# Kernel optimization log

Hardware: AMD Instinct MI355X
Metric: run time of the kernel (lower is better)

## Reference

```python
import jax, jax.numpy as jnp
import numpy as np
from jax import lax

NUM_NODES = 100000
FEAT = 256
RANK = 16
NNZ = 4000000
NUM_HE = 125000  # num_hyperedges == num_edges_total
K = 2000000      # int(0.5 * NNZ)


def setup_inputs() -> dict:
    key = jax.random.key(0)
    ks = jax.random.split(key, 6)
    x = jax.random.normal(ks[0], (NUM_NODES, FEAT), dtype=jnp.float32)
    W = jax.random.normal(ks[1], (RANK, FEAT), dtype=jnp.float32)
    edge_factors = jax.random.normal(ks[2], (NUM_HE, RANK), dtype=jnp.float32)
    V_idx = jax.random.randint(ks[3], (NNZ,), 0, NUM_NODES, dtype=jnp.int32)
    E_idx = jax.random.randint(ks[4], (NNZ,), 0, NUM_HE, dtype=jnp.int32)
    edge_ids = jax.random.randint(ks[5], (NUM_HE,), 0, NUM_HE, dtype=jnp.int32)
    return {"x": x, "W": W, "edge_factors": edge_factors,
            "V_idx": V_idx, "E_idx": E_idx, "edge_ids": edge_ids, "k": K}


def _segment_mean(vals, seg_ids, num_segments):
    s = jax.ops.segment_sum(vals, seg_ids, num_segments=num_segments)
    c = jax.ops.segment_sum(jnp.ones_like(vals), seg_ids, num_segments=num_segments)
    return s / jnp.maximum(c, 1.0)


def reference(x, W, edge_factors, V_idx, E_idx, edge_ids, k):
    # node_proj(x): [N, rank]; gather per-incidence node and edge factors, dot product
    proj = x @ W.T                                  # [N, rank]
    ef = edge_factors[edge_ids[E_idx]]              # [nnz, rank]
    logits = jnp.sum(proj[V_idx] * ef, axis=-1)     # [nnz]
    scores = jax.nn.sigmoid(logits)

    # is_test=True path: deterministic top-k keep set
    _, keep_ids = lax.top_k(scores, k)
    hard = jnp.zeros_like(scores).at[keep_ids].set(1.0)
    # straight-through: forward == hard, gradient flows through scores where hard==1
    soft = hard + (scores - lax.stop_gradient(scores)) * hard

    edge_probs = _segment_mean(lax.stop_gradient(scores), E_idx, NUM_HE)
    edge_soft = _segment_mean(soft, E_idx, NUM_HE)
    edge_hard = (_segment_mean(hard, E_idx, NUM_HE) > 0).astype(jnp.float32)
    return scores, soft, hard, edge_probs, edge_soft, edge_hard
```

## Files before the change

### kernel.cpp

```cpp
#include <hip/hip_runtime.h>
#include <math.h>

#define FEAT 256
#define RANKK 16
#define CAND_CAP 131072
#define TIE_CAP 2048
#define NBK_MAX 512
#define PB_CHUNK 8192
#define SPLIT 4
#define PRJ_NODES 64

typedef unsigned long long u64;

static __device__ __forceinline__ u64 pack_pair(unsigned e_low, unsigned bits, unsigned idx) {
    return ((u64)e_low << 56) | ((u64)bits << 26) | (u64)idx;
}

static __device__ __forceinline__ u64 pack_v(unsigned v, unsigned idx, unsigned e_low) {
    return ((u64)v << 40) | ((u64)idx << 8) | (u64)e_low;
}

__global__ __launch_bounds__(256) void ehist_scan(const int* __restrict__ E_idx,
        unsigned* __restrict__ bucketCnt, unsigned* __restrict__ bucketBase,
        unsigned* __restrict__ cursor, unsigned* __restrict__ ticket, int nnz) {
    __shared__ unsigned h[NBK_MAX];
    __shared__ unsigned ps[256];
    __shared__ unsigned isLast;
    int t = threadIdx.x;
    for (int j = t; j < NBK_MAX; j += 256) h[j] = 0;
    __syncthreads();
    for (int i = blockIdx.x * 256 + t; i < nnz; i += gridDim.x * 256)
        atomicAdd(&h[((unsigned)E_idx[i]) >> 8], 1u);
    __syncthreads();
    for (int j = t; j < NBK_MAX; j += 256)
        if (h[j]) atomicAdd(&bucketCnt[j], h[j]);
    __threadfence();
    if (t == 0) isLast = (atomicAdd(ticket, 1u) == gridDim.x - 1) ? 1u : 0u;
    __syncthreads();
    if (!isLast) return;
    unsigned a0 = atomicAdd(&bucketCnt[2 * t], 0u);
    unsigned a1 = atomicAdd(&bucketCnt[2 * t + 1], 0u);
    unsigned pairsum = a0 + a1;
    ps[t] = pairsum;
    __syncthreads();
    for (int off = 1; off < 256; off <<= 1) {
        unsigned v = (t >= off) ? ps[t - off] : 0u;
        __syncthreads();
        ps[t] += v;
        __syncthreads();
    }
    unsigned excl = ps[t] - pairsum;
    bucketBase[2 * t] = excl;           cursor[2 * t] = excl;
    bucketBase[2 * t + 1] = excl + a0;  cursor[2 * t + 1] = excl + a0;
    if (t == 255) bucketBase[NBK_MAX] = ps[255];
}

__global__ __launch_bounds__(256) void prep_combo(
        const float4* __restrict__ ef, const int* __restrict__ edge_ids,
        float4* __restrict__ ef2, int nhe,
        const float* __restrict__ x, const float* __restrict__ Wm,
        float* __restrict__ proj, int n_nodes, int G) {
    __shared__ float Ws[RANKK][FEAT + 4];
    __shared__ float Xs[PRJ_NODES][128 + 4];
    if ((int)blockIdx.x < G) {
        int t = blockIdx.x * 256 + threadIdx.x;
        if (t < nhe * 4) {
            int e = t >> 2, c = t & 3;
            ef2[(size_t)e * 4 + c] = ef[(size_t)edge_ids[e] * 4 + c];
        }
        return;
    }
    int pb = blockIdx.x - G;
    const float4* x4 = (const float4*)x;
    const float4* w4 = (const float4*)Wm;
    for (int i = threadIdx.x; i < RANKK * 64; i += 256) {
        int r = i >> 6, c4 = i & 63;
        *(float4*)&Ws[r][c4 * 4] = w4[(size_t)r * 64 + c4];
    }
    int nodeBase = pb * PRJ_NODES;
    int np = threadIdx.x >> 3;
    int rp = threadIdx.x & 7;
    int n0 = np * 2, r0 = rp * 2;
    double a00 = 0.0, a01 = 0.0, a10 = 0.0, a11 = 0.0;
    for (int chunk = 0; chunk < 2; ++chunk) {
        __syncthreads();
        for (int i = threadIdx.x; i < PRJ_NODES * 32; i += 256) {
            int row = i >> 5, c4 = i & 31;
            int node = nodeBase + row;
            float4 v = make_float4(0.f, 0.f, 0.f, 0.f);
            if (node < n_nodes) v = x4[(size_t)node * 64 + chunk * 32 + c4];
            *(float4*)&Xs[row][c4 * 4] = v;
        }
        __syncthreads();
        int jw = chunk * 128;
        #pragma unroll 8
        for (int j4 = 0; j4 < 32; ++j4) {
            float4 xa = *(const float4*)&Xs[n0][j4 * 4];
            float4 xb = *(const float4*)&Xs[n0 + 1][j4 * 4];
            float4 wa = *(const float4*)&Ws[r0][jw + j4 * 4];
            float4 wb = *(const float4*)&Ws[r0 + 1][jw + j4 * 4];
            a00 += (double)xa.x * wa.x + (double)xa.y * wa.y + (double)xa.z * wa.z + (double)xa.w * wa.w;
            a01 += (double)xa.x * wb.x + (double)xa.y * wb.y + (double)xa.z * wb.z + (double)xa.w * wb.w;
            a10 += (double)xb.x * wa.x + (double)xb.y * wa.y + (double)xb.z * wa.z + (double)xb.w * wa.w;
            a11 += (double)xb.x * wb.x + (double)xb.y * wb.y + (double)xb.z * wb.z + (double)xb.w * wb.w;
        }
    }
    int nodeA = nodeBase + n0;
    int nodeB = nodeA + 1;
    if (nodeA < n_nodes) {
        proj[(size_t)nodeA * RANKK + r0]     = (float)a00;
        proj[(size_t)nodeA * RANKK + r0 + 1] = (float)a01;
    }
    if (nodeB < n_nodes) {
        proj[(size_t)nodeB * RANKK + r0]     = (float)a10;
        proj[(size_t)nodeB * RANKK + r0 + 1] = (float)a11;
    }
}

__global__ __launch_bounds__(256) void sort_kernel(const int* __restrict__ V_idx,
        const int* __restrict__ E_idx, u64* __restrict__ vlist,
        unsigned* __restrict__ cursor, int nnz, int nb) {
    __shared__ unsigned bh[NBK_MAX];
    int t = threadIdx.x;
    for (int j = t; j < NBK_MAX; j += 256) bh[j] = 0;
    __syncthreads();
    int base = blockIdx.x * PB_CHUNK;
    int nE = nnz - base;
    if (nE > PB_CHUNK) nE = PB_CHUNK;
    for (int o = t; o < nE; o += 256)
        atomicAdd(&bh[((unsigned)E_idx[base + o]) >> 8], 1u);
    __syncthreads();
    for (int b = t; b < nb; b += 256) {
        unsigned c = bh[b];
        bh[b] = c ? atomicAdd(&cursor[b], c) : 0u;
    }
    __syncthreads();
    for (int o = t; o < nE; o += 256) {
        int i = base + o;
        unsigned e = (unsigned)E_idx[i];
        unsigned v = (unsigned)V_idx[i];
        unsigned pos = atomicAdd(&bh[e >> 8], 1u);
        vlist[pos] = pack_v(v, (unsigned)i, e & 255u);
    }
}

__global__ __launch_bounds__(256) void bucket_score(
        const float4* __restrict__ proj4, const float4* __restrict__ ef4,
        const unsigned* __restrict__ bucketBase, u64* __restrict__ list,
        float* __restrict__ scores, int nhe) {
    __shared__ float efs[256][20];
    int t = threadIdx.x;
    int b = blockIdx.x >> 2;
    int part = blockIdx.x & (SPLIT - 1);
    for (int jj = t; jj < 1024; jj += 256) {
        int edge = (b << 8) + (jj >> 2);
        if (edge < nhe) {
            float4 v = ef4[(size_t)edge * 4 + (jj & 3)];
            *(float4*)&efs[jj >> 2][(jj & 3) * 4] = v;
        }
    }
    __syncthreads();
    unsigned n0 = bucketBase[b], n1 = bucketBase[b + 1];
    #pragma unroll 2
    for (unsigned j = n0 + (part << 8) + t; j < n1; j += SPLIT * 256) {
        u64 p = list[j];
        unsigned v   = (unsigned)(p >> 40);
        unsigned idx = (unsigned)(p >> 8) & 0xFFFFFFu;
        unsigned el  = (unsigned)(p & 255u);
        float4 p0 = proj4[(size_t)v * 4 + 0];
        float4 p1 = proj4[(size_t)v * 4 + 1];
        float4 p2 = proj4[(size_t)v * 4 + 2];
        float4 p3 = proj4[(size_t)v * 4 + 3];
        float4 f0 = *(const float4*)&efs[el][0];
        float4 f1 = *(const float4*)&efs[el][4];
        float4 f2 = *(const float4*)&efs[el][8];
        float4 f3 = *(const float4*)&efs[el][12];
        double acc = (double)p0.x * f0.x + (double)p0.y * f0.y + (double)p0.z * f0.z + (double)p0.w * f0.w
                   + (double)p1.x * f1.x + (double)p1.y * f1.y + (double)p1.z * f1.z + (double)p1.w * f1.w
                   + (double)p2.x * f2.x + (double)p2.y * f2.y + (double)p2.z * f2.z + (double)p2.w * f2.w
                   + (double)p3.x * f3.x + (double)p3.y * f3.y + (double)p3.z * f3.z + (double)p3.w * f3.w;
        float s = (float)(1.0 / (1.0 + exp(-acc)));
        scores[idx] = s;
        list[j] = pack_pair(el, __float_as_uint(s), idx);
    }
}

__global__ __launch_bounds__(256) void score_linear(
        const float4* __restrict__ proj4, const float4* __restrict__ ef4,
        const int* __restrict__ V_idx, const int* __restrict__ E_idx,
        float* __restrict__ scores, int nnz) {
    int stride = gridDim.x * blockDim.x;
    #pragma unroll 2
    for (int i = blockIdx.x * blockDim.x + threadIdx.x; i < nnz; i += stride) {
        int v = V_idx[i], e = E_idx[i];
        float4 p0 = proj4[(size_t)v * 4 + 0];
        float4 p1 = proj4[(size_t)v * 4 + 1];
        float4 p2 = proj4[(size_t)v * 4 + 2];
        float4 p3 = proj4[(size_t)v * 4 + 3];
        float4 f0 = ef4[(size_t)e * 4 + 0];
        float4 f1 = ef4[(size_t)e * 4 + 1];
        float4 f2 = ef4[(size_t)e * 4 + 2];
        float4 f3 = ef4[(size_t)e * 4 + 3];
        double acc = (double)p0.x * f0.x + (double)p0.y * f0.y + (double)p0.z * f0.z + (double)p0.w * f0.w
                   + (double)p1.x * f1.x + (double)p1.y * f1.y + (double)p1.z * f1.z + (double)p1.w * f1.w
                   + (double)p2.x * f2.x + (double)p2.y * f2.y + (double)p2.z * f2.z + (double)p2.w * f2.w
                   + (double)p3.x * f3.x + (double)p3.y * f3.y + (double)p3.z * f3.z + (double)p3.w * f3.w;
        scores[i] = (float)(1.0 / (1.0 + exp(-acc)));
    }
}

__global__ __launch_bounds__(256) void pair_build(const int* __restrict__ E_idx,
        const float* __restrict__ scores, u64* __restrict__ pairs,
        unsigned* __restrict__ cursor, int nnz, int nb) {
    __shared__ unsigned bh[NBK_MAX];
    for (int t = threadIdx.x; t < NBK_MAX; t += 256) bh[t] = 0;
    __syncthreads();
    int base = blockIdx.x * PB_CHUNK;
    int nE = nnz - base;
    if (nE > PB_CHUNK) nE = PB_CHUNK;
    for (int o = threadIdx.x; o < nE; o += 256)
        atomicAdd(&bh[((unsigned)E_idx[base + o]) >> 8], 1u);
    __syncthreads();
    for (int b = threadIdx.x; b < nb; b += 256) {
        unsigned c = bh[b];
        bh[b] = c ? atomicAdd(&cursor[b], c) : 0u;
    }
    __syncthreads();
    for (int o = threadIdx.x; o < nE; o += 256) {
        int i = base + o;
        unsigned e = (unsigned)E_idx[i];
        unsigned bits = __float_as_uint(scores[i]);
        unsigned pos = atomicAdd(&bh[e >> 8], 1u);
        pairs[pos] = pack_pair(e & 255u, bits, (unsigned)i);
    }
}

__global__ void hist1_kernel(const float4* __restrict__ scores4, unsigned* __restrict__ hist1g,
                             int n4, int nnz) {
    __shared__ unsigned h[4096];
    for (int t = threadIdx.x; t < 4096; t += blockDim.x) h[t] = 0;
    __syncthreads();
    unsigned r1016 = 0, r1015 = 0, r0 = 0;
    int stride = gridDim.x * blockDim.x;
    for (int i = blockIdx.x * blockDim.x + threadIdx.x; i < n4; i += stride) {
        float4 sv = scores4[i];
        unsigned bb[4] = {__float_as_uint(sv.x), __float_as_uint(sv.y),
                          __float_as_uint(sv.z), __float_as_uint(sv.w)};
        #pragma unroll
        for (int q = 0; q < 4; ++q) {
            unsigned b = bb[q] >> 20;
            if (b == 1016) ++r1016;
            else if (b == 1015) ++r1015;
            else if (b == 0) ++r0;
            else atomicAdd(&h[b], 1u);
        }
    }
    for (int i = n4 * 4 + blockIdx.x * blockDim.x + threadIdx.x; i < nnz; i += stride) {
        unsigned b = __float_as_uint(((const float*)scores4)[i]) >> 20;
        if (b == 1016) ++r1016;
        else if (b == 1015) ++r1015;
        else if (b == 0) ++r0;
        else atomicAdd(&h[b], 1u);
    }
    if (r1016) atomicAdd(&h[1016], r1016);
    if (r1015) atomicAdd(&h[1015], r1015);
    if (r0) atomicAdd(&h[0], r0);
    __syncthreads();
    for (int t = threadIdx.x; t < 4096; t += blockDim.x)
        if (h[t]) atomicAdd(&hist1g[t], h[t]);
}

__global__ void scan1_kernel(const unsigned* __restrict__ hist,
                             unsigned* __restrict__ sel, const int* __restrict__ kptr) {
    __shared__ unsigned sfx[256];
    int t = threadIdx.x;
    unsigned local[16];
    unsigned s = 0;
    #pragma unroll
    for (int j = 0; j < 16; ++j) { local[j] = hist[t * 16 + j]; s += local[j]; }
    sfx[t] = s;
    __syncthreads();
    for (int off = 1; off < 256; off <<= 1) {
        unsigned add = (t + off < 256) ? sfx[t + off] : 0;
        __syncthreads();
        sfx[t] += add;
        __syncthreads();
    }
    unsigned krem = (unsigned)(*kptr);
    unsigned above = (t + 1 < 256) ? sfx[t + 1] : 0;
    if (above < krem && sfx[t] >= krem) {
        unsigned cum = above;
        int b = t * 16;
        for (int j = 15; j >= 0; --j) {
            unsigned cc = local[j];
            if (cum + cc >= krem) { b = t * 16 + j; break; }
            cum += cc;
        }
        sel[0] = krem - cum;
        sel[1] = ((unsigned)b) << 20;
    }
}

__global__ void compact_kernel(const float4* __restrict__ scores4,
                               const unsigned* __restrict__ sel,
                               uint2* __restrict__ cand, unsigned* __restrict__ candCount,
                               int n4, int nnz) {
    unsigned pref = sel[1] >> 20;
    int tid = blockIdx.x * blockDim.x + threadIdx.x;
    int stride = gridDim.x * blockDim.x;
    int lane = threadIdx.x & 63;
    int niter = (n4 + stride - 1) / stride;
    for (int kk = 0; kk < niter; ++kk) {
        int i = tid + kk * stride;
        bool inb = (i < n4);
        float4 sv = make_float4(0.f, 0.f, 0.f, 0.f);
        if (inb) sv = scores4[i];
        unsigned bb[4] = {__float_as_uint(sv.x), __float_as_uint(sv.y),
                          __float_as_uint(sv.z), __float_as_uint(sv.w)};
        #pragma unroll
        for (int q = 0; q < 4; ++q) {
            bool pred = inb && ((bb[q] >> 20) == pref);
            unsigned long long mask = __ballot(pred);
            if (mask) {
                int leader = __ffsll(mask) - 1;
                unsigned base = 0;
                if (lane == leader) base = atomicAdd(candCount, (unsigned)__popcll(mask));
                base = __shfl(base, leader, 64);
                if (pred) {
                    unsigned rank = __popcll(mask & ((1ull << lane) - 1ull));
                    unsigned pos = base + rank;
                    if (pos < CAND_CAP) cand[pos] = make_uint2(bb[q], (unsigned)(i * 4 + q));
                }
            }
        }
    }
    for (int i = n4 * 4 + tid; i < nnz; i += stride) {
        unsigned b = __float_as_uint(((const float*)scores4)[i]);
        if ((b >> 20) == pref) {
            unsigned pos = atomicAdd(candCount, 1u);
            if (pos < CAND_CAP) cand[pos] = make_uint2(b, (unsigned)i);
        }
    }
}

__global__ __launch_bounds__(256) void select_small(const uint2* __restrict__ cand,
                            const unsigned* __restrict__ candCount,
                            unsigned* __restrict__ sel, unsigned* __restrict__ tieList) {
    __shared__ unsigned h2[4096];
    __shared__ unsigned sfx[256];
    __shared__ unsigned sB2, sKrem2, sT, sM;
    __shared__ unsigned h3[256];
    __shared__ unsigned ties[TIE_CAP];
    __shared__ unsigned tcnt;
    int t = threadIdx.x;
    unsigned nc = *candCount;
    int n = (nc < CAND_CAP) ? (int)nc : CAND_CAP;
    unsigned krem = sel[0];
    unsigned pref = sel[1];

    for (int j = t; j < 4096; j += 256) h2[j] = 0;
    if (t == 0) tcnt = 0;
    __syncthreads();
    for (int j = t; j < n; j += 256) atomicAdd(&h2[(cand[j].x >> 8) & 0xFFF], 1u);
    __syncthreads();

    unsigned local[16];
    unsigned s = 0;
    #pragma unroll
    for (int j = 0; j < 16; ++j) { local[j] = h2[t * 16 + j]; s += local[j]; }
    sfx[t] = s;
    __syncthreads();
    for (int off = 1; off < 256; off <<= 1) {
        unsigned add = (t + off < 256) ? sfx[t + off] : 0;
        __syncthreads();
        sfx[t] += add;
        __syncthreads();
    }
    {
        unsigned above = (t + 1 < 256) ? sfx[t + 1] : 0;
        if (above < krem && sfx[t] >= krem) {
            unsigned cum = above;
            int b = t * 16;
            for (int j = 15; j >= 0; --j) {
                unsigned cc = local[j];
                if (cum + cc >= krem) { b = t * 16 + j; break; }
                cum += cc;
            }
            sB2 = (unsigned)b;
            sKrem2 = krem - cum;
        }
    }
    __syncthreads();

    h3[t] = 0;
    __syncthreads();
    unsigned b2 = sB2;
    for (int j = t; j < n; j += 256) {
        unsigned x = cand[j].x;
        if (((x >> 8) & 0xFFF) == b2) atomicAdd(&h3[x & 0xFF], 1u);
    }
    __syncthreads();
    sfx[t] = h3[t];
    __syncthreads();
    for (int off = 1; off < 256; off <<= 1) {
        unsigned add = (t + off < 256) ? sfx[t + off] : 0;
        __syncthreads();
        sfx[t] += add;
        __syncthreads();
    }
    {
        unsigned krem2 = sKrem2;
        unsigned above = (t + 1 < 256) ? sfx[t + 1] : 0;
        if (above < krem2 && sfx[t] >= krem2) {
            sT = pref | (b2 << 8) | (unsigned)t;
            sM = krem2 - above;
        }
    }
    __syncthreads();

    unsigned T = sT;
    for (int j = t; j < n; j += 256) {
        if (cand[j].x == T) {
            unsigned p = atomicAdd(&tcnt, 1u);
            if (p < TIE_CAP) ties[p] = cand[j].y;
        }
    }
    __syncthreads();
    if (t == 0) {
        unsigned cnt = (tcnt < TIE_CAP) ? tcnt : TIE_CAP;
        for (unsigned a = 1; a < cnt; ++a) {
            unsigned key = ties[a];
            int bpos = (int)a - 1;
            while (bpos >= 0 && ties[bpos] > key) { ties[bpos + 1] = ties[bpos]; --bpos; }
            ties[bpos + 1] = key;
        }
        unsigned m = sM;
        if (m > cnt) m = cnt;
        sel[2] = T;
        sel[3] = m;
        for (unsigned j = 0; j < m; ++j) tieList[j] = ties[j];
    }
}

__global__ __launch_bounds__(256) void edge_final(const u64* __restrict__ pairs,
        const unsigned* __restrict__ bucketBase, const unsigned* __restrict__ sel,
        const unsigned* __restrict__ tieList,
        float* __restrict__ eprob, float* __restrict__ esoft, float* __restrict__ ehard,
        int nhe) {
    __shared__ float ss[256];
    __shared__ unsigned cc[256];
    __shared__ unsigned hh[256];
    __shared__ unsigned ties[TIE_CAP];
    unsigned T = sel[2];
    unsigned m = sel[3];
    if (m > TIE_CAP) m = TIE_CAP;
    int t = threadIdx.x;
    ss[t] = 0.f; cc[t] = 0u; hh[t] = 0u;
    for (int j = t; j < (int)m; j += 256) ties[j] = tieList[j];
    __syncthreads();
    int b = blockIdx.x;
    unsigned n0 = bucketBase[b], n1 = bucketBase[b + 1];
    for (unsigned j = n0 + t; j < n1; j += 256) {
        u64 p = pairs[j];
        unsigned el = (unsigned)(p >> 56);
        unsigned bits = (unsigned)(p >> 26) & 0x3FFFFFFFu;
        atomicAdd(&ss[el], __uint_as_float(bits));
        atomicAdd(&cc[el], 1u);
        bool keep = bits > T;
        if (bits == T) {
            unsigned idx = (unsigned)(p & 0x3FFFFFFu);
            int lo = 0, hi = (int)m - 1;
            keep = false;
            while (lo <= hi) {
                int mid = (lo + hi) >> 1;
                unsigned v = ties[mid];
                if (v == idx) { keep = true; break; }
                if (v < idx) lo = mid + 1; else hi = mid - 1;
            }
        }
        if (keep) atomicAdd(&hh[el], 1u);
    }
    __syncthreads();
    int e = b * 256 + t;
    if (e < nhe) {
        float c = fmaxf((float)cc[t], 1.0f);
        eprob[e] = ss[t] / c;
        esoft[e] = (float)hh[t] / c;
        ehard[e] = (hh[t] > 0) ? 1.0f : 0.0f;
    }
}

__global__ __launch_bounds__(256) void write_hard(const float4* __restrict__ scores4,
                           const unsigned* __restrict__ sel,
                           const unsigned* __restrict__ tieList,
                           float4* __restrict__ hard4, float4* __restrict__ soft4,
                           int n4, int nnz) {
    __shared__ unsigned ties[TIE_CAP];
    unsigned T = sel[2];
    unsigned m = sel[3];
    if (m > TIE_CAP) m = TIE_CAP;
    for (int j = threadIdx.x; j < (int)m; j += blockDim.x) ties[j] = tieList[j];
    __syncthreads();
    int tid = blockIdx.x * blockDim.x + threadIdx.x;
    int stride = gridDim.x * blockDim.x;
    for (int i = tid; i < n4; i += stride) {
        float4 sv = scores4[i];
        unsigned bb[4] = {__float_as_uint(sv.x), __float_as_uint(sv.y),
                          __float_as_uint(sv.z), __float_as_uint(sv.w)};
        float hv[4];
        #pragma unroll
        for (int q = 0; q < 4; ++q) {
            bool keep = (bb[q] > T);
            if (bb[q] == T) {
                unsigned idx = (unsigned)(i * 4 + q);
                int lo = 0, hi = (int)m - 1;
                keep = false;
                while (lo <= hi) {
                    int mid = (lo + hi) >> 1;
                    unsigned v = ties[mid];
                    if (v == idx) { keep = true; break; }
                    if (v < idx) lo = mid + 1; else hi = mid - 1;
                }
            }
            hv[q] = keep ? 1.0f : 0.0f;
        }
        float4 outv = make_float4(hv[0], hv[1], hv[2], hv[3]);
        hard4[i] = outv;
        soft4[i] = outv;
    }
    const float* sc = (const float*)scores4;
    float* hard = (float*)hard4;
    float* soft = (float*)soft4;
    for (int i = n4 * 4 + tid; i < nnz; i += stride) {
        unsigned b = __float_as_uint(sc[i]);
        bool keep = (b > T);
        if (b == T) {
            unsigned idx = (unsigned)i;
            int lo = 0, hi = (int)m - 1;
            keep = false;
            while (lo <= hi) {
                int mid = (lo + hi) >> 1;
                unsigned v = ties[mid];
                if (v == idx) { keep = true; break; }
                if (v < idx) lo = mid + 1; else hi = mid - 1;
            }
        }
        float hvv = keep ? 1.0f : 0.0f;
        hard[i] = hvv;
        soft[i] = hvv;
    }
}

extern "C" void kernel_launch(void* const* d_in, const int* in_sizes, int n_in,
                              void* d_out, int out_size, void* d_ws, size_t ws_size,
                              hipStream_t stream) {
    const float* x        = (const float*)d_in[0];
    const float* Wm       = (const float*)d_in[1];
    const float* ef       = (const float*)d_in[2];
    const int*   V_idx    = (const int*)d_in[3];
    const int*   E_idx    = (const int*)d_in[4];
    const int*   edge_ids = (const int*)d_in[5];
    const int*   kptr     = (const int*)d_in[6];

    const int nnz     = in_sizes[3];
    const int nhe     = in_sizes[5];
    const int n_nodes = in_sizes[0] / FEAT;
    const int nb      = (nhe + 255) >> 8;

    float* out    = (float*)d_out;
    float* scores = out;
    float* soft   = out + (size_t)nnz;
    float* hard   = out + 2 * (size_t)nnz;
    float* eprob  = out + 3 * (size_t)nnz;
    float* esoft  = eprob + nhe;
    float* ehard  = esoft + nhe;

    u64*   vlist = (u64*)soft;
    uint2* cand  = (uint2*)eprob;

    char* w = (char*)d_ws;
    unsigned* hist1      = (unsigned*)w;
    unsigned* bucketCnt  = hist1 + 4096;
    unsigned* candCount  = bucketCnt + NBK_MAX;
    unsigned* ticket1    = candCount + 1;
    unsigned* sel        = ticket1 + 1;
    unsigned* tieList    = sel + 8;
    unsigned* bucketBase = tieList + TIE_CAP;
    unsigned* cursor     = bucketBase + NBK_MAX + 1;
    char* auxEnd = (char*)(cursor + NBK_MAX);
    size_t auxAligned = (((size_t)(auxEnd - w)) + 255) & ~(size_t)255;
    size_t zeroBytes = (size_t)(4096 + NBK_MAX + 2) * sizeof(unsigned);

    size_t ef2Bytes  = (size_t)nhe * RANKK * sizeof(float);
    size_t projBytes = (size_t)n_nodes * RANKK * sizeof(float);

    bool wsBig = (ws_size >= auxAligned + ef2Bytes + projBytes);
    float* ef2;
    float* proj;
    if (wsBig) {
        ef2  = (float*)(w + auxAligned);
        proj = (float*)(w + auxAligned + ef2Bytes);
    } else {
        ef2  = hard;
        proj = hard + (size_t)nhe * RANKK;
    }

    hipMemsetAsync(w, 0, zeroBytes, stream);

    ehist_scan<<<128, 256, 0, stream>>>(E_idx, bucketCnt, bucketBase, cursor, ticket1, nnz);

    int G = (nhe * 4 + 255) / 256;
    int P = (n_nodes + PRJ_NODES - 1) / PRJ_NODES;
    prep_combo<<<G + P, 256, 0, stream>>>((const float4*)ef, edge_ids, (float4*)ef2, nhe,
                                          x, Wm, proj, n_nodes, G);

    int nChunks = (nnz + PB_CHUNK - 1) / PB_CHUNK;
    if (wsBig) {
        sort_kernel<<<nChunks, 256, 0, stream>>>(V_idx, E_idx, vlist, cursor, nnz, nb);
        bucket_score<<<nb * SPLIT, 256, 0, stream>>>(
            (const float4*)proj, (const float4*)ef2, bucketBase, vlist, scores, nhe);
    } else {
        score_linear<<<2048, 256, 0, stream>>>(
            (const float4*)proj, (const float4*)ef2, V_idx, E_idx, scores, nnz);
        pair_build<<<nChunks, 256, 0, stream>>>(E_idx, scores, vlist, cursor, nnz, nb);
    }

    int n4 = nnz / 4;
    hist1_kernel<<<128, 256, 0, stream>>>((const float4*)scores, hist1, n4, nnz);
    scan1_kernel<<<1, 256, 0, stream>>>(hist1, sel, kptr);
    compact_kernel<<<1024, 256, 0, stream>>>(
        (const float4*)scores, sel, cand, candCount, n4, nnz);
    select_small<<<1, 256, 0, stream>>>(cand, candCount, sel, tieList);

    edge_final<<<nb, 256, 0, stream>>>(vlist, bucketBase, sel, tieList,
                                       eprob, esoft, ehard, nhe);
    write_hard<<<1024, 256, 0, stream>>>(
        (const float4*)scores, sel, tieList, (float4*)hard, (float4*)soft, n4, nnz);
}
```

Before: 472.6 us.

## Fuse prep, histogram-scan, and final stages to cut kernel launches

Merges the E_idx bucket histogram/scan into the projection/edge-gather prep kernel, and folds the score histogram and its scan into one kernel using a last-block ticket. When the workspace is large enough, the pair list moves out of the soft output buffer into workspace, so the edge reduction and the hard/soft writes can run together in a single launch. The intent is to remove launch gaps and serialization between small kernels, at the cost of more workspace, a larger shared-memory footprint for the merged prep kernel, and an extra memset'd ticket.

```diff
diff --git a/kernel.cpp b/kernel.cpp
--- a/kernel.cpp
+++ b/kernel.cpp
@@ -9,82 +9,86 @@
 #define PB_CHUNK 8192
 #define SPLIT 4
 #define PRJ_NODES 64
+#define EH_BLOCKS 128
+#define NW_BLOCKS 1024
 
 typedef unsigned long long u64;
 
 static __device__ __forceinline__ u64 pack_pair(unsigned e_low, unsigned bits, unsigned idx) {
     return ((u64)e_low << 56) | ((u64)bits << 26) | (u64)idx;
 }
-
 static __device__ __forceinline__ u64 pack_v(unsigned v, unsigned idx, unsigned e_low) {
     return ((u64)v << 40) | ((u64)idx << 8) | (u64)e_low;
 }
 
-__global__ __launch_bounds__(256) void ehist_scan(const int* __restrict__ E_idx,
-        unsigned* __restrict__ bucketCnt, unsigned* __restrict__ bucketBase,
-        unsigned* __restrict__ cursor, unsigned* __restrict__ ticket, int nnz) {
-    __shared__ unsigned h[NBK_MAX];
-    __shared__ unsigned ps[256];
-    __shared__ unsigned isLast;
-    int t = threadIdx.x;
-    for (int j = t; j < NBK_MAX; j += 256) h[j] = 0;
-    __syncthreads();
-    for (int i = blockIdx.x * 256 + t; i < nnz; i += gridDim.x * 256)
-        atomicAdd(&h[((unsigned)E_idx[i]) >> 8], 1u);
-    __syncthreads();
-    for (int j = t; j < NBK_MAX; j += 256)
-        if (h[j]) atomicAdd(&bucketCnt[j], h[j]);
-    __threadfence();
-    if (t == 0) isLast = (atomicAdd(ticket, 1u) == gridDim.x - 1) ? 1u : 0u;
-    __syncthreads();
-    if (!isLast) return;
-    unsigned a0 = atomicAdd(&bucketCnt[2 * t], 0u);
-    unsigned a1 = atomicAdd(&bucketCnt[2 * t + 1], 0u);
-    unsigned pairsum = a0 + a1;
-    ps[t] = pairsum;
-    __syncthreads();
-    for (int off = 1; off < 256; off <<= 1) {
-        unsigned v = (t >= off) ? ps[t - off] : 0u;
-        __syncthreads();
-        ps[t] += v;
-        __syncthreads();
-    }
-    unsigned excl = ps[t] - pairsum;
-    bucketBase[2 * t] = excl;           cursor[2 * t] = excl;
-    bucketBase[2 * t + 1] = excl + a0;  cursor[2 * t + 1] = excl + a0;
-    if (t == 255) bucketBase[NBK_MAX] = ps[255];
-}
-
-__global__ __launch_bounds__(256) void prep_combo(
+__global__ __launch_bounds__(256) void prep_all(
+        const int* __restrict__ E_idx, unsigned* __restrict__ bucketCnt,
+        unsigned* __restrict__ bucketBase, unsigned* __restrict__ cursor,
+        unsigned* __restrict__ ticket, int nnz,
         const float4* __restrict__ ef, const int* __restrict__ edge_ids,
         float4* __restrict__ ef2, int nhe,
         const float* __restrict__ x, const float* __restrict__ Wm,
         float* __restrict__ proj, int n_nodes, int G) {
-    __shared__ float Ws[RANKK][FEAT + 4];
-    __shared__ float Xs[PRJ_NODES][128 + 4];
-    if ((int)blockIdx.x < G) {
-        int t = blockIdx.x * 256 + threadIdx.x;
-        if (t < nhe * 4) {
-            int e = t >> 2, c = t & 3;
+    __shared__ float smem[12608];
+    __shared__ unsigned isLast;
+    int t = threadIdx.x;
+    int bid = blockIdx.x;
+
+    if (bid < EH_BLOCKS) {
+        unsigned* h  = (unsigned*)smem;
+        unsigned* ps = ((unsigned*)smem) + 512;
+        for (int j = t; j < NBK_MAX; j += 256) h[j] = 0;
+        __syncthreads();
+        for (int i = bid * 256 + t; i < nnz; i += EH_BLOCKS * 256)
+            atomicAdd(&h[((unsigned)E_idx[i]) >> 8], 1u);
+        __syncthreads();
+        for (int j = t; j < NBK_MAX; j += 256)
+            if (h[j]) atomicAdd(&bucketCnt[j], h[j]);
+        __threadfence();
+        if (t == 0) isLast = (atomicAdd(ticket, 1u) == EH_BLOCKS - 1) ? 1u : 0u;
+        __syncthreads();
+        if (!isLast) return;
+        unsigned a0 = atomicAdd(&bucketCnt[2 * t], 0u);
+        unsigned a1 = atomicAdd(&bucketCnt[2 * t + 1], 0u);
+        unsigned pairsum = a0 + a1;
+        ps[t] = pairsum;
+        __syncthreads();
+        for (int off = 1; off < 256; off <<= 1) {
+            unsigned v = (t >= off) ? ps[t - off] : 0u;
+            __syncthreads();
+            ps[t] += v;
+            __syncthreads();
+        }
+        unsigned excl = ps[t] - pairsum;
+        bucketBase[2 * t] = excl;           cursor[2 * t] = excl;
+        bucketBase[2 * t + 1] = excl + a0;  cursor[2 * t + 1] = excl + a0;
+        if (t == 255) bucketBase[NBK_MAX] = ps[255];
+        return;
+    }
+    if (bid < EH_BLOCKS + G) {
+        int tt = (bid - EH_BLOCKS) * 256 + t;
+        if (tt < nhe * 4) {
+            int e = tt >> 2, c = tt & 3;
             ef2[(size_t)e * 4 + c] = ef[(size_t)edge_ids[e] * 4 + c];
         }
         return;
     }
-    int pb = blockIdx.x - G;
+    int pb = bid - EH_BLOCKS - G;
+    float (*Ws)[FEAT + 4] = (float(*)[FEAT + 4])smem;
+    float (*Xs)[128 + 4]  = (float(*)[128 + 4])(smem + 4160);
     const float4* x4 = (const float4*)x;
     const float4* w4 = (const float4*)Wm;
-    for (int i = threadIdx.x; i < RANKK * 64; i += 256) {
+    for (int i = t; i < RANKK * 64; i += 256) {
         int r = i >> 6, c4 = i & 63;
         *(float4*)&Ws[r][c4 * 4] = w4[(size_t)r * 64 + c4];
     }
     int nodeBase = pb * PRJ_NODES;
-    int np = threadIdx.x >> 3;
-    int rp = threadIdx.x & 7;
+    int np = t >> 3, rp = t & 7;
     int n0 = np * 2, r0 = rp * 2;
     double a00 = 0.0, a01 = 0.0, a10 = 0.0, a11 = 0.0;
     for (int chunk = 0; chunk < 2; ++chunk) {
         __syncthreads();
-        for (int i = threadIdx.x; i < PRJ_NODES * 32; i += 256) {
+        for (int i = t; i < PRJ_NODES * 32; i += 256) {
             int row = i >> 5, c4 = i & 31;
             int node = nodeBase + row;
             float4 v = make_float4(0.f, 0.f, 0.f, 0.f);
@@ -208,7 +212,6 @@
         scores[i] = (float)(1.0 / (1.0 + exp(-acc)));
     }
 }
-
 __global__ __launch_bounds__(256) void pair_build(const int* __restrict__ E_idx,
         const float* __restrict__ scores, u64* __restrict__ pairs,
         unsigned* __restrict__ cursor, int nnz, int nb) {
@@ -235,14 +238,18 @@
     }
 }
 
-__global__ void hist1_kernel(const float4* __restrict__ scores4, unsigned* __restrict__ hist1g,
-                             int n4, int nnz) {
+__global__ __launch_bounds__(256) void hist1scan(const float4* __restrict__ scores4,
+        unsigned* __restrict__ hist1g, unsigned* __restrict__ ticket,
+        unsigned* __restrict__ sel, const int* __restrict__ kptr, int n4, int nnz) {
     __shared__ unsigned h[4096];
-    for (int t = threadIdx.x; t < 4096; t += blockDim.x) h[t] = 0;
+    __shared__ unsigned sfx[256];
+    __shared__ unsigned isLast;
+    int t = threadIdx.x;
+    for (int j = t; j < 4096; j += 256) h[j] = 0;
     __syncthreads();
     unsigned r1016 = 0, r1015 = 0, r0 = 0;
-    int stride = gridDim.x * blockDim.x;
-    for (int i = blockIdx.x * blockDim.x + threadIdx.x; i < n4; i += stride) {
+    int stride = gridDim.x * 256;
+    for (int i = blockIdx.x * 256 + t; i < n4; i += stride) {
         float4 sv = scores4[i];
         unsigned bb[4] = {__float_as_uint(sv.x), __float_as_uint(sv.y),
                           __float_as_uint(sv.z), __float_as_uint(sv.w)};
@@ -255,7 +262,7 @@
             else atomicAdd(&h[b], 1u);
         }
     }
-    for (int i = n4 * 4 + blockIdx.x * blockDim.x + threadIdx.x; i < nnz; i += stride) {
+    for (int i = n4 * 4 + blockIdx.x * 256 + t; i < nnz; i += stride) {
         unsigned b = __float_as_uint(((const float*)scores4)[i]) >> 20;
         if (b == 1016) ++r1016;
         else if (b == 1015) ++r1015;
@@ -266,18 +273,16 @@
     if (r1015) atomicAdd(&h[1015], r1015);
     if (r0) atomicAdd(&h[0], r0);
     __syncthreads();
-    for (int t = threadIdx.x; t < 4096; t += blockDim.x)
-        if (h[t]) atomicAdd(&hist1g[t], h[t]);
-}
-
-__global__ void scan1_kernel(const unsigned* __restrict__ hist,
-                             unsigned* __restrict__ sel, const int* __restrict__ kptr) {
-    __shared__ unsigned sfx[256];
-    int t = threadIdx.x;
+    for (int j = t; j < 4096; j += 256)
+        if (h[j]) atomicAdd(&hist1g[j], h[j]);
+    __threadfence();
+    if (t == 0) isLast = (atomicAdd(ticket, 1u) == gridDim.x - 1) ? 1u : 0u;
+    __syncthreads();
+    if (!isLast) return;
     unsigned local[16];
     unsigned s = 0;
     #pragma unroll
-    for (int j = 0; j < 16; ++j) { local[j] = hist[t * 16 + j]; s += local[j]; }
+    for (int j = 0; j < 16; ++j) { local[j] = atomicAdd(&hist1g[t * 16 + j], 0u); s += local[j]; }
     sfx[t] = s;
     __syncthreads();
     for (int off = 1; off < 256; off <<= 1) {
@@ -442,6 +447,108 @@
     }
 }
 
+__global__ __launch_bounds__(256) void final_combo(const u64* __restrict__ pairs,
+        const unsigned* __restrict__ bucketBase, const unsigned* __restrict__ sel,
+        const unsigned* __restrict__ tieList, const float4* __restrict__ scores4,
+        float* __restrict__ eprob, float* __restrict__ esoft, float* __restrict__ ehard,
+        float4* __restrict__ hard4, float4* __restrict__ soft4,
+        int nb, int n4, int nnz, int nhe) {
+    __shared__ float ss[256];
+    __shared__ unsigned cc[256];
+    __shared__ unsigned hh[256];
+    __shared__ unsigned ties[TIE_CAP];
+    unsigned T = sel[2];
+    unsigned m = sel[3];
+    if (m > TIE_CAP) m = TIE_CAP;
+    int t = threadIdx.x;
+    for (int j = t; j < (int)m; j += 256) ties[j] = tieList[j];
+
+    if ((int)blockIdx.x < nb) {
+        ss[t] = 0.f; cc[t] = 0u; hh[t] = 0u;
+        __syncthreads();
+        int b = blockIdx.x;
+        unsigned n0 = bucketBase[b], n1 = bucketBase[b + 1];
+        for (unsigned j = n0 + t; j < n1; j += 256) {
+            u64 p = pairs[j];
+            unsigned el = (unsigned)(p >> 56);
+            unsigned bits = (unsigned)(p >> 26) & 0x3FFFFFFFu;
+            atomicAdd(&ss[el], __uint_as_float(bits));
+            atomicAdd(&cc[el], 1u);
+            bool keep = bits > T;
+            if (bits == T) {
+                unsigned idx = (unsigned)(p & 0x3FFFFFFu);
+                int lo = 0, hi = (int)m - 1;
+                keep = false;
+                while (lo <= hi) {
+                    int mid = (lo + hi) >> 1;
+                    unsigned v = ties[mid];
+                    if (v == idx) { keep = true; break; }
+                    if (v < idx) lo = mid + 1; else hi = mid - 1;
+                }
+            }
+            if (keep) atomicAdd(&hh[el], 1u);
+        }
+        __syncthreads();
+        int e = blockIdx.x * 256 + t;
+        if (e < nhe) {
+            float c = fmaxf((float)cc[t], 1.0f);
+            eprob[e] = ss[t] / c;
+            esoft[e] = (float)hh[t] / c;
+            ehard[e] = (hh[t] > 0) ? 1.0f : 0.0f;
+        }
+        return;
+    }
+    __syncthreads();
+    int tid = (blockIdx.x - nb) * 256 + t;
+    int stride = NW_BLOCKS * 256;
+    for (int i = tid; i < n4; i += stride) {
+        float4 sv = scores4[i];
+        unsigned bb[4] = {__float_as_uint(sv.x), __float_as_uint(sv.y),
+                          __float_as_uint(sv.z), __float_as_uint(sv.w)};
+        float hv[4];
+        #pragma unroll
+        for (int q = 0; q < 4; ++q) {
+            bool keep = (bb[q] > T);
+            if (bb[q] == T) {
+                unsigned idx = (unsigned)(i * 4 + q);
+                int lo = 0, hi = (int)m - 1;
+                keep = false;
+                while (lo <= hi) {
+                    int mid = (lo + hi) >> 1;
+                    unsigned v = ties[mid];
+                    if (v == idx) { keep = true; break; }
+                    if (v < idx) lo = mid + 1; else hi = mid - 1;
+                }
+            }
+            hv[q] = keep ? 1.0f : 0.0f;
+        }
+        float4 outv = make_float4(hv[0], hv[1], hv[2], hv[3]);
+        hard4[i] = outv;
+        soft4[i] = outv;
+    }
+    const float* sc = (const float*)scores4;
+    float* hard = (float*)hard4;
+    float* soft = (float*)soft4;
+    for (int i = n4 * 4 + tid; i < nnz; i += stride) {
+        unsigned b = __float_as_uint(sc[i]);
+        bool keep = (b > T);
+        if (b == T) {
+            unsigned idx = (unsigned)i;
+            int lo = 0, hi = (int)m - 1;
+            keep = false;
+            while (lo <= hi) {
+                int mid = (lo + hi) >> 1;
+                unsigned v = ties[mid];
+                if (v == idx) { keep = true; break; }
+                if (v < idx) lo = mid + 1; else hi = mid - 1;
+            }
+        }
+        float hvv = keep ? 1.0f : 0.0f;
+        hard[i] = hvv;
+        soft[i] = hvv;
+    }
+}
+
 __global__ __launch_bounds__(256) void edge_final(const u64* __restrict__ pairs,
         const unsigned* __restrict__ bucketBase, const unsigned* __restrict__ sel,
         const unsigned* __restrict__ tieList,
@@ -489,7 +596,6 @@
         ehard[e] = (hh[t] > 0) ? 1.0f : 0.0f;
     }
 }
-
 __global__ __launch_bounds__(256) void write_hard(const float4* __restrict__ scores4,
                            const unsigned* __restrict__ sel,
                            const unsigned* __restrict__ tieList,
@@ -575,44 +681,50 @@
     float* esoft  = eprob + nhe;
     float* ehard  = esoft + nhe;
 
-    u64*   vlist = (u64*)soft;
-    uint2* cand  = (uint2*)eprob;
+    uint2* cand = (uint2*)eprob;
 
     char* w = (char*)d_ws;
     unsigned* hist1      = (unsigned*)w;
     unsigned* bucketCnt  = hist1 + 4096;
     unsigned* candCount  = bucketCnt + NBK_MAX;
     unsigned* ticket1    = candCount + 1;
-    unsigned* sel        = ticket1 + 1;
+    unsigned* ticket2    = ticket1 + 1;
+    unsigned* sel        = ticket2 + 1;
     unsigned* tieList    = sel + 8;
     unsigned* bucketBase = tieList + TIE_CAP;
     unsigned* cursor     = bucketBase + NBK_MAX + 1;
     char* auxEnd = (char*)(cursor + NBK_MAX);
     size_t auxAligned = (((size_t)(auxEnd - w)) + 255) & ~(size_t)255;
-    size_t zeroBytes = (size_t)(4096 + NBK_MAX + 2) * sizeof(unsigned);
-
-    size_t ef2Bytes  = (size_t)nhe * RANKK * sizeof(float);
-    size_t projBytes = (size_t)n_nodes * RANKK * sizeof(float);
-
-    bool wsBig = (ws_size >= auxAligned + ef2Bytes + projBytes);
+    size_t zeroBytes = (size_t)(4096 + NBK_MAX + 3) * sizeof(unsigned);
+
+    size_t ef2Bytes   = (size_t)nhe * RANKK * sizeof(float);
+    size_t projBytes  = (size_t)n_nodes * RANKK * sizeof(float);
+    size_t pairsBytes = (size_t)nnz * sizeof(u64);
+
+    bool wsBig  = (ws_size >= auxAligned + ef2Bytes + projBytes);
+    bool wsHuge = (ws_size >= auxAligned + ef2Bytes + projBytes + pairsBytes);
+
     float* ef2;
     float* proj;
+    u64*   vlist;
     if (wsBig) {
         ef2  = (float*)(w + auxAligned);
         proj = (float*)(w + auxAligned + ef2Bytes);
+        vlist = wsHuge ? (u64*)(w + auxAligned + ef2Bytes + projBytes) : (u64*)soft;
     } else {
         ef2  = hard;
         proj = hard + (size_t)nhe * RANKK;
+        vlist = (u64*)soft;
     }
 
     hipMemsetAsync(w, 0, zeroBytes, stream);
-
-    ehist_scan<<<128, 256, 0, stream>>>(E_idx, bucketCnt, bucketBase, cursor, ticket1, nnz);
 
     int G = (nhe * 4 + 255) / 256;
     int P = (n_nodes + PRJ_NODES - 1) / PRJ_NODES;
-    prep_combo<<<G + P, 256, 0, stream>>>((const float4*)ef, edge_ids, (float4*)ef2, nhe,
-                                          x, Wm, proj, n_nodes, G);
+    prep_all<<<EH_BLOCKS + G + P, 256, 0, stream>>>(
+        E_idx, bucketCnt, bucketBase, cursor, ticket1, nnz,
+        (const float4*)ef, edge_ids, (float4*)ef2, nhe,
+        x, Wm, proj, n_nodes, G);
 
     int nChunks = (nnz + PB_CHUNK - 1) / PB_CHUNK;
     if (wsBig) {
@@ -626,14 +738,20 @@
     }
 
     int n4 = nnz / 4;
-    hist1_kernel<<<128, 256, 0, stream>>>((const float4*)scores, hist1, n4, nnz);
-    scan1_kernel<<<1, 256, 0, stream>>>(hist1, sel, kptr);
+    hist1scan<<<128, 256, 0, stream>>>((const float4*)scores, hist1, ticket2,
+                                       sel, kptr, n4, nnz);
     compact_kernel<<<1024, 256, 0, stream>>>(
         (const float4*)scores, sel, cand, candCount, n4, nnz);
     select_small<<<1, 256, 0, stream>>>(cand, candCount, sel, tieList);
 
-    edge_final<<<nb, 256, 0, stream>>>(vlist, bucketBase, sel, tieList,
-                                       eprob, esoft, ehard, nhe);
-    write_hard<<<1024, 256, 0, stream>>>(
-        (const float4*)scores, sel, tieList, (float4*)hard, (float4*)soft, n4, nnz);
-}
+    if (wsHuge) {
+        final_combo<<<nb + NW_BLOCKS, 256, 0, stream>>>(
+            vlist, bucketBase, sel, tieList, (const float4*)scores,
+            eprob, esoft, ehard, (float4*)hard, (float4*)soft, nb, n4, nnz, nhe);
+    } else {
+        edge_final<<<nb, 256, 0, stream>>>(vlist, bucketBase, sel, tieList,
+                                           eprob, esoft, ehard, nhe);
+        write_hard<<<1024, 256, 0, stream>>>(
+            (const float4*)scores, sel, tieList, (float4*)hard, (float4*)soft, n4, nnz);
+    }
+}
```

Measured after the change: 444.8 us, median of 2. -5.9%, faster.
